# Optimization experiments

Hardware: AMD Instinct MI355X
Metric: run time of the kernel (lower is better)

## Reference

```python
import jax, jax.numpy as jnp
import numpy as np

N, E, F_IN, HID, H, NC, G = 50000, 800000, 128, 64, 4, 64, 128
EPS_BN = 1e-5


def setup_inputs() -> dict:
    key = jax.random.key(0)
    ks = jax.random.split(key, 32)
    inp = {}
    inp['x'] = jax.random.normal(ks[0], (N, F_IN), dtype=jnp.float32)
    inp['edge_index'] = jax.random.randint(ks[1], (2, E), 0, N, dtype=jnp.int32)
    inp['batch'] = jnp.sort(jax.random.randint(ks[2], (N,), 0, G, dtype=jnp.int32))
    dims = [(F_IN, HID, H, True), (HID * H, HID, H, True), (HID * H, NC, 1, False)]
    k = 3
    for li, (fin, c, h, concat) in enumerate(dims):
        out_flat = c * h if concat else c
        inp[f'W{li}'] = jax.random.normal(ks[k], (fin, h * c), dtype=jnp.float32) * (1.0 / np.sqrt(fin)); k += 1
        inp[f'asrc{li}'] = jax.random.normal(ks[k], (h, c), dtype=jnp.float32) * 0.1; k += 1
        inp[f'adst{li}'] = jax.random.normal(ks[k], (h, c), dtype=jnp.float32) * 0.1; k += 1
        inp[f'b{li}'] = jnp.zeros((out_flat,), dtype=jnp.float32)
        inp[f'gamma{li}'] = jnp.ones((out_flat,), dtype=jnp.float32)
        inp[f'beta{li}'] = jnp.zeros((out_flat,), dtype=jnp.float32)
    return inp


def gat_layer(x, src, dst, W, asrc, adst, b, heads, out_ch, concat):
    n = x.shape[0]
    h = (x @ W).reshape(n, heads, out_ch)                      # [N,H,C]
    a_s = jnp.sum(h * asrc, axis=-1)                           # [N,H]
    a_d = jnp.sum(h * adst, axis=-1)                           # [N,H]
    e = jax.nn.leaky_relu(a_s[src] + a_d[dst], 0.2)            # [E',H]
    m = jax.ops.segment_max(e, dst, num_segments=n)            # per-target max
    e = jnp.exp(e - m[dst])
    s = jax.ops.segment_sum(e, dst, num_segments=n)
    alpha = e / (s[dst] + 1e-16)                               # softmax over in-edges
    msg = alpha[:, :, None] * h[src]                           # [E',H,C]
    out = jax.ops.segment_sum(msg, dst, num_segments=n)        # [N,H,C]
    out = out.reshape(n, heads * out_ch) if concat else out.mean(axis=1)
    return out + b


def batchnorm(x, gamma, beta):
    mu = x.mean(axis=0)
    var = x.var(axis=0)  # biased, as torch BN training-mode
    return (x - mu) * jax.lax.rsqrt(var + EPS_BN) * gamma + beta


def reference(x, edge_index, batch, W0, asrc0, adst0, b0, gamma0, beta0,
              W1, asrc1, adst1, b1, gamma1, beta1,
              W2, asrc2, adst2, b2, gamma2, beta2):
    n = x.shape[0]
    loop = jnp.arange(n, dtype=edge_index.dtype)
    src = jnp.concatenate([edge_index[0], loop])  # add self loops (PyG default)
    dst = jnp.concatenate([edge_index[1], loop])
    layers = [(W0, asrc0, adst0, b0, gamma0, beta0, H, HID, True),
              (W1, asrc1, adst1, b1, gamma1, beta1, H, HID, True),
              (W2, asrc2, adst2, b2, gamma2, beta2, 1, NC, False)]
    xs = []
    for (W, asrc, adst, b, gamma, beta, heads, oc, concat) in layers:
        x = jax.nn.elu(gat_layer(x, src, dst, W, asrc, adst, b, heads, oc, concat))
        x = batchnorm(x, gamma, beta)
        xs.append(x)
    x_pool = jnp.concatenate([jax.ops.segment_sum(xx, batch, num_segments=G) for xx in xs], axis=1)
    return (x_pool, jnp.concatenate(xs, axis=1))
```

## Files before the change

kernel.cpp:

```cpp
#include <hip/hip_runtime.h>
#include <math.h>

#define N_NODES 50000
#define NUM_E   800000
#define E_TOT   (NUM_E + N_NODES)
#define M_PAD   50048
#define NGRAPH  128
#define XS_COLS 576
#define EPS_BN  1e-5f

static inline int ceil_div(int a, int b) { return (a + b - 1) / b; }

typedef __attribute__((ext_vector_type(8))) short short8;
typedef __attribute__((ext_vector_type(4))) float f32x4;

__device__ __forceinline__ float bf2f(ushort u) {
    union { unsigned int i; float f; } v; v.i = ((unsigned int)u) << 16; return v.f;
}
__device__ __forceinline__ ushort f2bf(float f) {
    union { float f; unsigned int i; } v; v.f = f;
    unsigned int r = v.i + 0x7FFF + ((v.i >> 16) & 1);
    return (ushort)(r >> 16);
}
__device__ __forceinline__ float lrelu(float l) { return l > 0.f ? l : 0.2f * l; }

__global__ __launch_bounds__(256)
void prep_w(const float* __restrict__ W0, const float* __restrict__ W1,
            const float* __restrict__ W2,
            ushort* __restrict__ Wt0, ushort* __restrict__ Wt1, ushort* __restrict__ Wt2)
{
    int j = blockIdx.x * 256 + threadIdx.x;
    if (j < 256 * 128) { Wt0[j] = f2bf(W0[(size_t)(j % 128) * 256 + (j / 128)]); return; }
    j -= 256 * 128;
    if (j < 256 * 256) { Wt1[j] = f2bf(W1[(size_t)(j % 256) * 256 + (j / 256)]); return; }
    j -= 256 * 256;
    if (j < 64 * 256)  { Wt2[j] = f2bf(W2[(size_t)(j % 256) * 64 + (j / 256)]); }
}

template<bool AF32>
__global__ __launch_bounds__(512)
void gemm_bf16_w(const void* __restrict__ Av, int lda,
                 const ushort* __restrict__ Bt, int ldb,
                 ushort* __restrict__ C, int M, int K,
                 const float* __restrict__ asrc, const float* __restrict__ adst,
                 float* __restrict__ a_s, float* __restrict__ a_d)
{
    __shared__ __align__(16) ushort As[128][64 + 8];
    __shared__ __align__(16) ushort Bs[256][64 + 8];
    const int tid = threadIdx.x;
    const int lane = tid & 63;
    const int w = tid >> 6;
    const int m0 = blockIdx.x * 128;

    f32x4 acc[16] = {};

    for (int k0 = 0; k0 < K; k0 += 64) {
#pragma unroll
        for (int j = 0; j < 2; ++j) {
            int c = tid + j * 512;
            int r = c >> 3, cc = (c & 7) * 8;
            if constexpr (AF32) {
                const float* Af = (const float*)Av;
                int m = m0 + r; if (m >= M) m = M - 1;
                float4 v0 = *reinterpret_cast<const float4*>(Af + (size_t)m * lda + k0 + cc);
                float4 v1 = *reinterpret_cast<const float4*>(Af + (size_t)m * lda + k0 + cc + 4);
                short8 v = {(short)f2bf(v0.x), (short)f2bf(v0.y), (short)f2bf(v0.z), (short)f2bf(v0.w),
                            (short)f2bf(v1.x), (short)f2bf(v1.y), (short)f2bf(v1.z), (short)f2bf(v1.w)};
                *reinterpret_cast<short8*>(&As[r][cc]) = v;
            } else {
                const ushort* Ab = (const ushort*)Av;
                short8 v = *reinterpret_cast<const short8*>(Ab + (size_t)(m0 + r) * lda + k0 + cc);
                *reinterpret_cast<short8*>(&As[r][cc]) = v;
            }
        }
#pragma unroll
        for (int j = 0; j < 4; ++j) {
            int c = tid + j * 512;
            int r = c >> 3, cc = (c & 7) * 8;
            short8 v = *reinterpret_cast<const short8*>(Bt + (size_t)r * ldb + k0 + cc);
            *reinterpret_cast<short8*>(&Bs[r][cc]) = v;
        }
        __syncthreads();
#pragma unroll
        for (int kc = 0; kc < 64; kc += 32) {
            short8 a = *reinterpret_cast<const short8*>(&As[w * 16 + (lane & 15)][kc + (lane >> 4) * 8]);
#pragma unroll
            for (int nf = 0; nf < 16; ++nf) {
                short8 b = *reinterpret_cast<const short8*>(&Bs[nf * 16 + (lane & 15)][kc + (lane >> 4) * 8]);
                acc[nf] = __builtin_amdgcn_mfma_f32_16x16x32_bf16(a, b, acc[nf], 0, 0, 0);
            }
        }
        __syncthreads();
    }

    const int mbase = m0 + w * 16 + (lane >> 4) * 4;
#pragma unroll
    for (int r = 0; r < 4; ++r) {
        int m = mbase + r;
        if (m < M) {
#pragma unroll
            for (int nf = 0; nf < 16; ++nf)
                C[(size_t)m * 256 + nf * 16 + (lane & 15)] = f2bf(acc[nf][r]);
        }
    }

    float asl[16], adl[16];
#pragma unroll
    for (int nf = 0; nf < 16; ++nf) {
        int col = nf * 16 + (lane & 15);
        asl[nf] = asrc[col];
        adl[nf] = adst[col];
    }
#pragma unroll
    for (int r = 0; r < 4; ++r) {
        float ps[4] = {0.f, 0.f, 0.f, 0.f};
        float pd[4] = {0.f, 0.f, 0.f, 0.f};
#pragma unroll
        for (int nf = 0; nf < 16; ++nf) {
            int h = nf >> 2;
            ps[h] = fmaf(acc[nf][r], asl[nf], ps[h]);
            pd[h] = fmaf(acc[nf][r], adl[nf], pd[h]);
        }
#pragma unroll
        for (int h = 0; h < 4; ++h) {
#pragma unroll
            for (int o = 1; o < 16; o <<= 1) {
                ps[h] += __shfl_xor(ps[h], o, 64);
                pd[h] += __shfl_xor(pd[h], o, 64);
            }
        }
        int m = mbase + r;
        if ((lane & 15) == 0 && m < M) {
#pragma unroll
            for (int h = 0; h < 4; ++h) {
                a_s[(size_t)m * 4 + h] = ps[h];
                a_d[(size_t)m * 4 + h] = pd[h];
            }
        }
    }
}

template<int BM, int BN, int BK, int H>
__global__ __launch_bounds__(256)
void gemm_bf16(const ushort* __restrict__ A, int lda,
               const ushort* __restrict__ Bt, int ldb,
               ushort* __restrict__ C, int ldc, int M, int K,
               const float* __restrict__ asrc, const float* __restrict__ adst,
               float* __restrict__ a_s, float* __restrict__ a_d)
{
    static_assert(BM == 128 && BN == 64 && BK == 64, "tuned variant");
    __shared__ __align__(16) ushort As[BM][BK + 8];
    __shared__ __align__(16) ushort Bs[BN][BK + 8];
    const int tid = threadIdx.x;
    const int lane = tid & 63;
    const int w = tid >> 6;
    const int m0 = blockIdx.x * BM;
    const int n0 = blockIdx.y * BN;

    f32x4 acc[2][4] = {};

    for (int k0 = 0; k0 < K; k0 += BK) {
#pragma unroll
        for (int j = 0; j < 4; ++j) {
            int c = tid + j * 256;
            int r = c >> 3, cc = (c & 7) * 8;
            short8 v = *reinterpret_cast<const short8*>(A + (size_t)(m0 + r) * lda + k0 + cc);
            *reinterpret_cast<short8*>(&As[r][cc]) = v;
        }
#pragma unroll
        for (int j = 0; j < 2; ++j) {
            int c = tid + j * 256;
            int r = c >> 3, cc = (c & 7) * 8;
            short8 v = *reinterpret_cast<const short8*>(Bt + (size_t)(n0 + r) * ldb + k0 + cc);
            *reinterpret_cast<short8*>(&Bs[r][cc]) = v;
        }
        __syncthreads();
#pragma unroll
        for (int kc = 0; kc < BK; kc += 32) {
            short8 a[2], b[4];
#pragma unroll
            for (int mf = 0; mf < 2; ++mf)
                a[mf] = *reinterpret_cast<const short8*>(&As[w * 32 + mf * 16 + (lane & 15)][kc + (lane >> 4) * 8]);
#pragma unroll
            for (int nf = 0; nf < 4; ++nf)
                b[nf] = *reinterpret_cast<const short8*>(&Bs[nf * 16 + (lane & 15)][kc + (lane >> 4) * 8]);
#pragma unroll
            for (int mf = 0; mf < 2; ++mf)
#pragma unroll
                for (int nf = 0; nf < 4; ++nf)
                    acc[mf][nf] = __builtin_amdgcn_mfma_f32_16x16x32_bf16(a[mf], b[nf], acc[mf][nf], 0, 0, 0);
        }
        __syncthreads();
    }

#pragma unroll
    for (int mf = 0; mf < 2; ++mf) {
        int mbase = m0 + w * 32 + mf * 16 + (lane >> 4) * 4;
#pragma unroll
        for (int r = 0; r < 4; ++r) {
            int m = mbase + r;
            if (m < M) {
#pragma unroll
                for (int nf = 0; nf < 4; ++nf)
                    C[(size_t)m * ldc + n0 + nf * 16 + (lane & 15)] = f2bf(acc[mf][nf][r]);
            }
        }
    }

    const int hd = blockIdx.y;
    float asl[4], adl[4];
#pragma unroll
    for (int nf = 0; nf < 4; ++nf) {
        int col = n0 + nf * 16 + (lane & 15);
        asl[nf] = asrc[col];
        adl[nf] = adst[col];
    }
#pragma unroll
    for (int mf = 0; mf < 2; ++mf) {
#pragma unroll
        for (int r = 0; r < 4; ++r) {
            float ps = 0.f, pd = 0.f;
#pragma unroll
            for (int nf = 0; nf < 4; ++nf) {
                ps = fmaf(acc[mf][nf][r], asl[nf], ps);
                pd = fmaf(acc[mf][nf][r], adl[nf], pd);
            }
#pragma unroll
            for (int o = 1; o < 16; o <<= 1) {
                ps += __shfl_xor(ps, o, 64);
                pd += __shfl_xor(pd, o, 64);
            }
            int m = m0 + w * 32 + mf * 16 + (lane >> 4) * 4 + r;
            if ((lane & 15) == 0 && m < M) {
                a_s[(size_t)m * H + hd] = ps;
                a_d[(size_t)m * H + hd] = pd;
            }
        }
    }
}

template<int H, int C>
__global__ __launch_bounds__(256)
void gat_fused2(const int* __restrict__ offs, const int* __restrict__ ssrc,
                const float* __restrict__ a_s, const float* __restrict__ a_d,
                const ushort* __restrict__ hf, const float* __restrict__ bias,
                float* __restrict__ out, int ldo)
{
    constexpr int V = (H * C) / 32;
    __shared__ float alsh[4][2][64 * H];
    __shared__ int   ssh[4][2][64];
    const int tid = threadIdx.x;
    const int lane = tid & 63;
    const int wv = tid >> 6;
    const int half = lane >> 5;
    const int ll = lane & 31;
    const int dst = blockIdx.x * 8 + wv * 2 + half;
    if (dst >= N_NODES) return;
    const int e0 = offs[dst], e1 = offs[dst + 1];
    const int deg = e1 - e0;
    const int hd = (ll * V) / C;

    float ad[H];
    if constexpr (H == 4) {
        float4 v = *reinterpret_cast<const float4*>(a_d + (size_t)dst * 4);
        ad[0] = v.x; ad[1] = v.y; ad[2] = v.z; ad[3] = v.w;
    } else ad[0] = a_d[dst];

    float acc[V];
#pragma unroll
    for (int k = 0; k < V; ++k) acc[k] = 0.f;

    if (deg <= 64) {
        const bool a0 = ll < deg;
        const bool a1 = 32 + ll < deg;
        const int s0 = ssrc[e0 + (a0 ? ll : 0)];
        const int s1 = ssrc[e0 + (a1 ? 32 + ll : 0)];
        float l0[H], l1[H], mx[H], sm[H];
        if constexpr (H == 4) {
            float4 v0 = *reinterpret_cast<const float4*>(a_s + (size_t)s0 * 4);
            float4 v1 = *reinterpret_cast<const float4*>(a_s + (size_t)s1 * 4);
            l0[0] = lrelu(v0.x + ad[0]); l0[1] = lrelu(v0.y + ad[1]);
            l0[2] = lrelu(v0.z + ad[2]); l0[3] = lrelu(v0.w + ad[3]);
            l1[0] = lrelu(v1.x + ad[0]); l1[1] = lrelu(v1.y + ad[1]);
            l1[2] = lrelu(v1.z + ad[2]); l1[3] = lrelu(v1.w + ad[3]);
        } else {
            l0[0] = lrelu(a_s[s0] + ad[0]);
            l1[0] = lrelu(a_s[s1] + ad[0]);
        }
#pragma unroll
        for (int t = 0; t < H; ++t) {
            float m = a0 ? l0[t] : -INFINITY;
            if (a1) m = fmaxf(m, l1[t]);
#pragma unroll
            for (int o = 1; o < 32; o <<= 1) m = fmaxf(m, __shfl_xor(m, o, 64));
            mx[t] = m;
            float s = (a0 ? __expf(l0[t] - m) : 0.f) + (a1 ? __expf(l1[t] - m) : 0.f);
#pragma unroll
            for (int o = 1; o < 32; o <<= 1) s += __shfl_xor(s, o, 64);
            sm[t] = s;
        }
        float inv[H];
#pragma unroll
        for (int t = 0; t < H; ++t) inv[t] = 1.f / (sm[t] + 1e-16f);
        if (a0) {
            ssh[wv][half][ll] = s0;
            if constexpr (H == 4) {
                float4 av = {__expf(l0[0] - mx[0]) * inv[0], __expf(l0[1] - mx[1]) * inv[1],
                             __expf(l0[2] - mx[2]) * inv[2], __expf(l0[3] - mx[3]) * inv[3]};
                *reinterpret_cast<float4*>(&alsh[wv][half][ll * 4]) = av;
            } else alsh[wv][half][ll] = __expf(l0[0] - mx[0]) * inv[0];
        }
        if (a1) {
            ssh[wv][half][32 + ll] = s1;
            if constexpr (H == 4) {
                float4 av = {__expf(l1[0] - mx[0]) * inv[0], __expf(l1[1] - mx[1]) * inv[1],
                             __expf(l1[2] - mx[2]) * inv[2], __expf(l1[3] - mx[3]) * inv[3]};
                *reinterpret_cast<float4*>(&alsh[wv][half][(32 + ll) * 4]) = av;
            } else alsh[wv][half][32 + ll] = __expf(l1[0] - mx[0]) * inv[0];
        }

        const ushort* hlane = hf + (size_t)ll * V;
        int j = 0;
        for (; j + 3 < deg; j += 4) {
            int sj[4]; float al[4];
#pragma unroll
            for (int k = 0; k < 4; ++k) {
                sj[k] = ssh[wv][half][j + k];
                al[k] = alsh[wv][half][(j + k) * H + hd];
            }
            if constexpr (V == 8) {
                short8 hv[4];
#pragma unroll
                for (int k = 0; k < 4; ++k)
                    hv[k] = *reinterpret_cast<const short8*>(hlane + (size_t)sj[k] * (H * C));
#pragma unroll
                for (int k = 0; k < 4; ++k)
#pragma unroll
                    for (int i = 0; i < 8; ++i)
                        acc[i] = fmaf(al[k], bf2f((ushort)hv[k][i]), acc[i]);
            } else {
                ushort2 hv[4];
#pragma unroll
                for (int k = 0; k < 4; ++k)
                    hv[k] = *reinterpret_cast<const ushort2*>(hlane + (size_t)sj[k] * (H * C));
#pragma unroll
                for (int k = 0; k < 4; ++k) {
                    acc[0] = fmaf(al[k], bf2f(hv[k].x), acc[0]);
                    acc[1] = fmaf(al[k], bf2f(hv[k].y), acc[1]);
                }
            }
        }
        for (; j < deg; ++j) {
            int sj = ssh[wv][half][j];
            float al = alsh[wv][half][j * H + hd];
            if constexpr (V == 8) {
                short8 hv = *reinterpret_cast<const short8*>(hlane + (size_t)sj * (H * C));
#pragma unroll
                for (int i = 0; i < 8; ++i)
                    acc[i] = fmaf(al, bf2f((ushort)hv[i]), acc[i]);
            } else {
                ushort2 hv = *reinterpret_cast<const ushort2*>(hlane + (size_t)sj * (H * C));
                acc[0] = fmaf(al, bf2f(hv.x), acc[0]);
                acc[1] = fmaf(al, bf2f(hv.y), acc[1]);
            }
        }
    } else {
        float mx[H], sm[H];
#pragma unroll
        for (int t = 0; t < H; ++t) mx[t] = -INFINITY;
        for (int e = e0 + ll; e < e1; e += 32) {
            int s = ssrc[e];
            float asv[H];
            if constexpr (H == 4) {
                float4 v = *reinterpret_cast<const float4*>(a_s + (size_t)s * 4);
                asv[0] = v.x; asv[1] = v.y; asv[2] = v.z; asv[3] = v.w;
            } else asv[0] = a_s[s];
#pragma unroll
            for (int t = 0; t < H; ++t) mx[t] = fmaxf(mx[t], lrelu(asv[t] + ad[t]));
        }
#pragma unroll
        for (int t = 0; t < H; ++t)
#pragma unroll
            for (int o = 1; o < 32; o <<= 1) mx[t] = fmaxf(mx[t], __shfl_xor(mx[t], o, 64));
#pragma unroll
        for (int t = 0; t < H; ++t) sm[t] = 0.f;
        for (int e = e0 + ll; e < e1; e += 32) {
            int s = ssrc[e];
            float asv[H];
            if constexpr (H == 4) {
                float4 v = *reinterpret_cast<const float4*>(a_s + (size_t)s * 4);
                asv[0] = v.x; asv[1] = v.y; asv[2] = v.z; asv[3] = v.w;
            } else asv[0] = a_s[s];
#pragma unroll
            for (int t = 0; t < H; ++t) sm[t] += __expf(lrelu(asv[t] + ad[t]) - mx[t]);
        }
#pragma unroll
        for (int t = 0; t < H; ++t)
#pragma unroll
            for (int o = 1; o < 32; o <<= 1) sm[t] += __shfl_xor(sm[t], o, 64);

        float mxl = mx[0], sml = sm[0], adl = ad[0];
#pragma unroll
        for (int t = 1; t < H; ++t) {
            mxl = (hd == t) ? mx[t] : mxl;
            sml = (hd == t) ? sm[t] : sml;
            adl = (hd == t) ? ad[t] : adl;
        }
        const float invl = 1.f / (sml + 1e-16f);
        const ushort* hlane = hf + (size_t)ll * V;
        for (int e = e0; e < e1; ++e) {
            int s0 = ssrc[e];
            float al0 = __expf(lrelu(a_s[(size_t)s0 * H + hd] + adl) - mxl) * invl;
            if constexpr (V == 8) {
                short8 hv = *reinterpret_cast<const short8*>(hlane + (size_t)s0 * (H * C));
#pragma unroll
                for (int i = 0; i < 8; ++i)
                    acc[i] = fmaf(al0, bf2f((ushort)hv[i]), acc[i]);
            } else {
                ushort2 hv = *reinterpret_cast<const ushort2*>(hlane + (size_t)s0 * (H * C));
                acc[0] = fmaf(al0, bf2f(hv.x), acc[0]);
                acc[1] = fmaf(al0, bf2f(hv.y), acc[1]);
            }
        }
    }

    float res[V];
#pragma unroll
    for (int i = 0; i < V; ++i) {
        float t = acc[i] + bias[ll * V + i];
        res[i] = t > 0.f ? t : (expf(t) - 1.f);
    }
    if constexpr (V == 8) {
        float4 v0 = {res[0], res[1], res[2], res[3]};
        float4 v1 = {res[4], res[5], res[6], res[7]};
        *reinterpret_cast<float4*>(&out[(size_t)dst * ldo + ll * 8 + 0]) = v0;
        *reinterpret_cast<float4*>(&out[(size_t)dst * ldo + ll * 8 + 4]) = v1;
    } else {
        float2 v = {res[0], res[1]};
        *reinterpret_cast<float2*>(&out[(size_t)dst * ldo + ll * 2]) = v;
    }
}

__global__ void edge_count(const int* __restrict__ ei, int* __restrict__ counts)
{
    int i = blockIdx.x * blockDim.x + threadIdx.x;
    if (i >= E_TOT) return;
    int dst = (i < NUM_E) ? ei[NUM_E + i] : (i - NUM_E);
    atomicAdd(&counts[dst], 1);
}

__global__ void edge_scatter(const int* __restrict__ ei, int* __restrict__ cursor,
                             int* __restrict__ ssrc)
{
    int i = blockIdx.x * blockDim.x + threadIdx.x;
    if (i >= E_TOT) return;
    int src, dst;
    if (i < NUM_E) { src = ei[i]; dst = ei[NUM_E + i]; }
    else           { src = dst = i - NUM_E; }
    int pos = atomicAdd(&cursor[dst], 1);
    ssrc[pos] = src;
}

__global__ void scan_block(const int* __restrict__ in, int n,
                           int* __restrict__ incl, int* __restrict__ bsum)
{
    __shared__ int sh[256];
    int tid = threadIdx.x;
    int i = blockIdx.x * 256 + tid;
    int v = (i < n) ? in[i] : 0;
    sh[tid] = v;
    __syncthreads();
    for (int o = 1; o < 256; o <<= 1) {
        int t = (tid >= o) ? sh[tid - o] : 0;
        __syncthreads();
        sh[tid] += t;
        __syncthreads();
    }
    if (i < n) incl[i] = sh[tid];
    if (tid == 255) bsum[blockIdx.x] = sh[255];
}

__global__ void scan_sums(int* __restrict__ bsum, int nb)
{
    __shared__ int sh[256];
    int tid = threadIdx.x;
    int v = (tid < nb) ? bsum[tid] : 0;
    sh[tid] = v;
    __syncthreads();
    for (int o = 1; o < 256; o <<= 1) {
        int t = (tid >= o) ? sh[tid - o] : 0;
        __syncthreads();
        sh[tid] += t;
        __syncthreads();
    }
    if (tid < nb) bsum[tid] = sh[tid] - v;
}

__global__ void scan_final(const int* __restrict__ incl, const int* __restrict__ in,
                           const int* __restrict__ bsum, int n,
                           int* __restrict__ offs, int* __restrict__ cursor)
{
    int i = blockIdx.x * 256 + threadIdx.x;
    if (i >= n) return;
    int excl = incl[i] - in[i] + bsum[i / 256];
    offs[i] = excl;
    cursor[i] = excl;
    if (i == n - 1) offs[n] = incl[i] + bsum[i / 256];
}

template<int OF>
__global__ __launch_bounds__(256)
void bn_stats(const float* __restrict__ x, int ldx, float* __restrict__ part)
{
    constexpr int RP = 256 / OF;
    const int tid = threadIdx.x;
    const int col = tid % OF;
    const int rsub = tid / OF;
    float s = 0.f, s2 = 0.f;
    for (int r = blockIdx.x * RP + rsub; r < N_NODES; r += gridDim.x * RP) {
        float v = x[(size_t)r * ldx + col];
        s += v;
        s2 = fmaf(v, v, s2);
    }
    if constexpr (RP > 1) {
        __shared__ float sh[2][256];
        sh[0][tid] = s; sh[1][tid] = s2;
        __syncthreads();
        if (rsub == 0) {
#pragma unroll
            for (int j = 1; j < RP; ++j) { s += sh[0][col + j * OF]; s2 += sh[1][col + j * OF]; }
        }
    }
    if (rsub == 0) {
        part[(size_t)blockIdx.x * 2 * OF + col] = s;
        part[(size_t)blockIdx.x * 2 * OF + OF + col] = s2;
    }
}

template<int OF>
__global__ void bn_finalize(const float* __restrict__ part, const float* __restrict__ gamma,
                            const float* __restrict__ beta, float* __restrict__ ss)
{
    int c = threadIdx.x;
    if (c >= OF) return;
    float s = 0.f, s2 = 0.f;
    for (int b = 0; b < 256; ++b) {
        s += part[(size_t)b * 2 * OF + c];
        s2 += part[(size_t)b * 2 * OF + OF + c];
    }
    float mean = s / (float)N_NODES;
    float var = s2 / (float)N_NODES - mean * mean;
    float inv = rsqrtf(var + EPS_BN);
    float sc = inv * gamma[c];
    ss[c] = sc;
    ss[OF + c] = beta[c] - mean * sc;
}

template<int OF, bool WB>
__global__ __launch_bounds__(256)
void bn_apply_pool(float* __restrict__ x, int ldx, const float* __restrict__ ss,
                   ushort* __restrict__ xb, int ldxb,
                   const int* __restrict__ batch, float* __restrict__ pool, int poff)
{
    const int tid = threadIdx.x;
    if constexpr (OF == 256) {
        const int c = tid;
        const int r0 = blockIdx.x * 16;
        const float sc = ss[c], sh = ss[OF + c];
        float psum = 0.f;
        int curg = batch[r0];
#pragma unroll
        for (int i = 0; i < 16; ++i) {
            int r = r0 + i;
            int g = batch[r];
            if (g != curg) {
                atomicAdd(&pool[(size_t)curg * XS_COLS + poff + c], psum);
                psum = 0.f; curg = g;
            }
            float v = fmaf(x[(size_t)r * ldx + c], sc, sh);
            x[(size_t)r * ldx + c] = v;
            if constexpr (WB) xb[(size_t)r * ldxb + c] = f2bf(v);
            psum += v;
        }
        atomicAdd(&pool[(size_t)curg * XS_COLS + poff + c], psum);
    } else {
        const int c = tid & 63;
        const int rsub = tid >> 6;
        const int r0 = blockIdx.x * 16;
        const float sc = ss[c], sh = ss[OF + c];
        float psum = 0.f;
        int curg = batch[r0 + rsub];
#pragma unroll
        for (int i = 0; i < 4; ++i) {
            int r = r0 + rsub + i * 4;
            int g = batch[r];
            if (g != curg) {
                atomicAdd(&pool[(size_t)curg * XS_COLS + poff + c], psum);
                psum = 0.f; curg = g;
            }
            float v = fmaf(x[(size_t)r * ldx + c], sc, sh);
            x[(size_t)r * ldx + c] = v;
            if constexpr (WB) xb[(size_t)r * ldxb + c] = f2bf(v);
            psum += v;
        }
        atomicAdd(&pool[(size_t)curg * XS_COLS + poff + c], psum);
    }
}

extern "C" void kernel_launch(void* const* d_in, const int* in_sizes, int n_in,
                              void* d_out, int out_size, void* d_ws, size_t ws_size,
                              hipStream_t stream)
{
    const float* x     = (const float*)d_in[0];
    const int*   ei    = (const int*)d_in[1];
    const int*   batch = (const int*)d_in[2];
    const float* W[3]    = {(const float*)d_in[3],  (const float*)d_in[9],  (const float*)d_in[15]};
    const float* asrc[3] = {(const float*)d_in[4],  (const float*)d_in[10], (const float*)d_in[16]};
    const float* adst[3] = {(const float*)d_in[5],  (const float*)d_in[11], (const float*)d_in[17]};
    const float* bia[3]  = {(const float*)d_in[6],  (const float*)d_in[12], (const float*)d_in[18]};
    const float* gam[3]  = {(const float*)d_in[7],  (const float*)d_in[13], (const float*)d_in[19]};
    const float* bet[3]  = {(const float*)d_in[8],  (const float*)d_in[14], (const float*)d_in[20]};

    char* wp = (char*)d_ws;
    auto alloc = [&](size_t bytes) -> void* {
        void* p = (void*)wp;
        wp += (bytes + 255) & ~(size_t)255;
        return p;
    };
    ushort* hbf   = (ushort*)alloc((size_t)N_NODES * 256 * 2);
    ushort* AbfA  = (ushort*)alloc((size_t)M_PAD * 256 * 2);
    float*  a_s   = (float*)alloc((size_t)N_NODES * 4 * 4);
    float*  a_d   = (float*)alloc((size_t)N_NODES * 4 * 4);
    int*    counts = (int*)alloc((size_t)N_NODES * 4);
    int*    offs   = (int*)alloc((size_t)(N_NODES + 1) * 4);
    int*    cursor = (int*)alloc((size_t)N_NODES * 4);
    int*    incl   = (int*)alloc((size_t)N_NODES * 4);
    int*    bsums  = (int*)alloc(1024);
    int*    ssrc   = (int*)alloc((size_t)E_TOT * 4);
    float*  bnpart = (float*)alloc((size_t)256 * 2 * 256 * 4);
    float*  bnss   = (float*)alloc(2 * 256 * 4);
    ushort* Wt0    = (ushort*)alloc(256 * 128 * 2);
    ushort* Wt1    = (ushort*)alloc(256 * 256 * 2);
    ushort* Wt2    = (ushort*)alloc(64 * 256 * 2);

    float* pool = (float*)d_out;
    float* xs   = pool + (size_t)NGRAPH * XS_COLS;

    hipMemsetAsync(counts, 0, (size_t)N_NODES * 4, stream);
    hipMemsetAsync(pool, 0, (size_t)NGRAPH * XS_COLS * 4, stream);
    edge_count<<<ceil_div(E_TOT, 256), 256, 0, stream>>>(ei, counts);
    const int NSB = ceil_div(N_NODES, 256);
    scan_block<<<NSB, 256, 0, stream>>>(counts, N_NODES, incl, bsums);
    scan_sums<<<1, 256, 0, stream>>>(bsums, NSB);
    scan_final<<<NSB, 256, 0, stream>>>(incl, counts, bsums, N_NODES, offs, cursor);
    edge_scatter<<<ceil_div(E_TOT, 256), 256, 0, stream>>>(ei, cursor, ssrc);
    const int PREP_ITEMS = 256 * 128 + 256 * 256 + 64 * 256;
    prep_w<<<ceil_div(PREP_ITEMS, 256), 256, 0, stream>>>(W[0], W[1], W[2], Wt0, Wt1, Wt2);

    const int NW2 = ceil_div(N_NODES, 8);
    const int NMB = ceil_div(N_NODES, 128);
    const int NBA = N_NODES / 16;

    {
        gemm_bf16_w<true><<<NMB, 512, 0, stream>>>(x, 128, Wt0, 128, hbf, N_NODES, 128,
                                                   asrc[0], adst[0], a_s, a_d);
        gat_fused2<4, 64><<<NW2, 256, 0, stream>>>(offs, ssrc, a_s, a_d, hbf, bia[0], xs + 0, XS_COLS);
        bn_stats<256><<<256, 256, 0, stream>>>(xs + 0, XS_COLS, bnpart);
        bn_finalize<256><<<1, 256, 0, stream>>>(bnpart, gam[0], bet[0], bnss);
        bn_apply_pool<256, true><<<NBA, 256, 0, stream>>>(xs + 0, XS_COLS, bnss, AbfA, 256,
                                                          batch, pool, 0);
    }
    {
        gemm_bf16_w<false><<<NMB, 512, 0, stream>>>(AbfA, 256, Wt1, 256, hbf, N_NODES, 256,
                                                    asrc[1], adst[1], a_s, a_d);
        gat_fused2<4, 64><<<NW2, 256, 0, stream>>>(offs, ssrc, a_s, a_d, hbf, bia[1], xs + 256, XS_COLS);
        bn_stats<256><<<256, 256, 0, stream>>>(xs + 256, XS_COLS, bnpart);
        bn_finalize<256><<<1, 256, 0, stream>>>(bnpart, gam[1], bet[1], bnss);
        bn_apply_pool<256, true><<<NBA, 256, 0, stream>>>(xs + 256, XS_COLS, bnss, AbfA, 256,
                                                          batch, pool, 256);
    }
    {
        dim3 grid(NMB, 1);
        gemm_bf16<128, 64, 64, 1><<<grid, 256, 0, stream>>>(AbfA, 256, Wt2, 256, hbf, 64, N_NODES, 256,
                                                            asrc[2], adst[2], a_s, a_d);
        gat_fused2<1, 64><<<NW2, 256, 0, stream>>>(offs, ssrc, a_s, a_d, hbf, bia[2], xs + 512, XS_COLS);
        bn_stats<64><<<256, 256, 0, stream>>>(xs + 512, XS_COLS, bnpart);
        bn_finalize<64><<<1, 64, 0, stream>>>(bnpart, gam[2], bet[2], bnss);
        bn_apply_pool<64, false><<<NBA, 256, 0, stream>>>(xs + 512, XS_COLS, bnss, nullptr, 0,
                                                          batch, pool, 512);
    }
}
```

Before: 532.8 us.

## Fuse BN statistics into GAT aggregation, stage activations in bf16, merge scan kernels

The GAT aggregation kernel now writes its ELU output as bf16 to a scratch buffer and accumulates per-column sum and sum-of-squares through shared memory. It then issues atomics into 8 slotted partial buffers, which removes the separate bn_stats pass over the fp32 activations. bn_apply_pool reads the bf16 buffer, vectorised two columns per thread, and writes the fp32 output. The scan_sums kernel is folded into scan_final, which reduces the block sums itself. The cost is extra memsets, atomic contention across 8 slots, and BN normalisation applied to bf16-rounded values, which costs precision. The early return for out-of-range dst is also removed, which is safe here because N is a multiple of 8.

```diff
diff --git a/kernel.cpp b/kernel.cpp
--- a/kernel.cpp
+++ b/kernel.cpp
@@ -244,18 +244,20 @@
 void gat_fused2(const int* __restrict__ offs, const int* __restrict__ ssrc,
                 const float* __restrict__ a_s, const float* __restrict__ a_d,
                 const ushort* __restrict__ hf, const float* __restrict__ bias,
-                float* __restrict__ out, int ldo)
+                ushort* __restrict__ ybuf, float* __restrict__ bnsum)
 {
     constexpr int V = (H * C) / 32;
+    constexpr int OF = H * C;
     __shared__ float alsh[4][2][64 * H];
     __shared__ int   ssh[4][2][64];
+    __shared__ float ysh[8][OF];
     const int tid = threadIdx.x;
     const int lane = tid & 63;
     const int wv = tid >> 6;
     const int half = lane >> 5;
     const int ll = lane & 31;
-    const int dst = blockIdx.x * 8 + wv * 2 + half;
-    if (dst >= N_NODES) return;
+    const int dl = wv * 2 + half;
+    const int dst = blockIdx.x * 8 + dl;
     const int e0 = offs[dst], e1 = offs[dst + 1];
     const int deg = e1 - e0;
     const int hd = (ll * V) / C;
@@ -332,7 +334,7 @@
                 short8 hv[4];
 #pragma unroll
                 for (int k = 0; k < 4; ++k)
-                    hv[k] = *reinterpret_cast<const short8*>(hlane + (size_t)sj[k] * (H * C));
+                    hv[k] = *reinterpret_cast<const short8*>(hlane + (size_t)sj[k] * OF);
 #pragma unroll
                 for (int k = 0; k < 4; ++k)
 #pragma unroll
@@ -342,7 +344,7 @@
                 ushort2 hv[4];
 #pragma unroll
                 for (int k = 0; k < 4; ++k)
-                    hv[k] = *reinterpret_cast<const ushort2*>(hlane + (size_t)sj[k] * (H * C));
+                    hv[k] = *reinterpret_cast<const ushort2*>(hlane + (size_t)sj[k] * OF);
 #pragma unroll
                 for (int k = 0; k < 4; ++k) {
                     acc[0] = fmaf(al[k], bf2f(hv[k].x), acc[0]);
@@ -354,12 +356,12 @@
             int sj = ssh[wv][half][j];
             float al = alsh[wv][half][j * H + hd];
             if constexpr (V == 8) {
-                short8 hv = *reinterpret_cast<const short8*>(hlane + (size_t)sj * (H * C));
+                short8 hv = *reinterpret_cast<const short8*>(hlane + (size_t)sj * OF);
 #pragma unroll
                 for (int i = 0; i < 8; ++i)
                     acc[i] = fmaf(al, bf2f((ushort)hv[i]), acc[i]);
             } else {
-                ushort2 hv = *reinterpret_cast<const ushort2*>(hlane + (size_t)sj * (H * C));
+                ushort2 hv = *reinterpret_cast<const ushort2*>(hlane + (size_t)sj * OF);
                 acc[0] = fmaf(al, bf2f(hv.x), acc[0]);
                 acc[1] = fmaf(al, bf2f(hv.y), acc[1]);
             }
@@ -412,12 +414,12 @@
             int s0 = ssrc[e];
             float al0 = __expf(lrelu(a_s[(size_t)s0 * H + hd] + adl) - mxl) * invl;
             if constexpr (V == 8) {
-                short8 hv = *reinterpret_cast<const short8*>(hlane + (size_t)s0 * (H * C));
+                short8 hv = *reinterpret_cast<const short8*>(hlane + (size_t)s0 * OF);
 #pragma unroll
                 for (int i = 0; i < 8; ++i)
                     acc[i] = fmaf(al0, bf2f((ushort)hv[i]), acc[i]);
             } else {
-                ushort2 hv = *reinterpret_cast<const ushort2*>(hlane + (size_t)s0 * (H * C));
+                ushort2 hv = *reinterpret_cast<const ushort2*>(hlane + (size_t)s0 * OF);
                 acc[0] = fmaf(al0, bf2f(hv.x), acc[0]);
                 acc[1] = fmaf(al0, bf2f(hv.y), acc[1]);
             }
@@ -431,13 +433,29 @@
         res[i] = t > 0.f ? t : (expf(t) - 1.f);
     }
     if constexpr (V == 8) {
-        float4 v0 = {res[0], res[1], res[2], res[3]};
-        float4 v1 = {res[4], res[5], res[6], res[7]};
-        *reinterpret_cast<float4*>(&out[(size_t)dst * ldo + ll * 8 + 0]) = v0;
-        *reinterpret_cast<float4*>(&out[(size_t)dst * ldo + ll * 8 + 4]) = v1;
+        short8 yv = {(short)f2bf(res[0]), (short)f2bf(res[1]), (short)f2bf(res[2]), (short)f2bf(res[3]),
+                     (short)f2bf(res[4]), (short)f2bf(res[5]), (short)f2bf(res[6]), (short)f2bf(res[7])};
+        *reinterpret_cast<short8*>(&ybuf[(size_t)dst * OF + ll * 8]) = yv;
+        *reinterpret_cast<f32x4*>(&ysh[dl][ll * 8 + 0]) = f32x4{res[0], res[1], res[2], res[3]};
+        *reinterpret_cast<f32x4*>(&ysh[dl][ll * 8 + 4]) = f32x4{res[4], res[5], res[6], res[7]};
     } else {
-        float2 v = {res[0], res[1]};
-        *reinterpret_cast<float2*>(&out[(size_t)dst * ldo + ll * 2]) = v;
+        ushort2 yv = {f2bf(res[0]), f2bf(res[1])};
+        *reinterpret_cast<ushort2*>(&ybuf[(size_t)dst * OF + ll * 2]) = yv;
+        ysh[dl][ll * 2 + 0] = res[0];
+        ysh[dl][ll * 2 + 1] = res[1];
+    }
+    __syncthreads();
+    if (tid < OF) {
+        float s = 0.f, s2 = 0.f;
+#pragma unroll
+        for (int d = 0; d < 8; ++d) {
+            float v = ysh[d][tid];
+            s += v;
+            s2 = fmaf(v, v, s2);
+        }
+        int slot = blockIdx.x & 7;
+        atomicAdd(&bnsum[(size_t)slot * 2 * OF + tid], s);
+        atomicAdd(&bnsum[(size_t)slot * 2 * OF + OF + tid], s2);
     }
 }
 
@@ -480,73 +498,39 @@
     if (tid == 255) bsum[blockIdx.x] = sh[255];
 }
 
-__global__ void scan_sums(int* __restrict__ bsum, int nb)
-{
-    __shared__ int sh[256];
-    int tid = threadIdx.x;
-    int v = (tid < nb) ? bsum[tid] : 0;
-    sh[tid] = v;
-    __syncthreads();
-    for (int o = 1; o < 256; o <<= 1) {
-        int t = (tid >= o) ? sh[tid - o] : 0;
-        __syncthreads();
-        sh[tid] += t;
-        __syncthreads();
-    }
-    if (tid < nb) bsum[tid] = sh[tid] - v;
-}
-
 __global__ void scan_final(const int* __restrict__ incl, const int* __restrict__ in,
                            const int* __restrict__ bsum, int n,
                            int* __restrict__ offs, int* __restrict__ cursor)
 {
-    int i = blockIdx.x * 256 + threadIdx.x;
+    __shared__ int sh[256];
+    const int tid = threadIdx.x;
+    const int bi = blockIdx.x;
+    sh[tid] = (tid < bi) ? bsum[tid] : 0;
+    __syncthreads();
+    for (int o = 128; o > 0; o >>= 1) {
+        if (tid < o) sh[tid] += sh[tid + o];
+        __syncthreads();
+    }
+    const int pref = sh[0];
+    int i = bi * 256 + tid;
     if (i >= n) return;
-    int excl = incl[i] - in[i] + bsum[i / 256];
+    int excl = incl[i] - in[i] + pref;
     offs[i] = excl;
     cursor[i] = excl;
-    if (i == n - 1) offs[n] = incl[i] + bsum[i / 256];
+    if (i == n - 1) offs[n] = incl[i] + pref;
 }
 
 template<int OF>
-__global__ __launch_bounds__(256)
-void bn_stats(const float* __restrict__ x, int ldx, float* __restrict__ part)
-{
-    constexpr int RP = 256 / OF;
-    const int tid = threadIdx.x;
-    const int col = tid % OF;
-    const int rsub = tid / OF;
-    float s = 0.f, s2 = 0.f;
-    for (int r = blockIdx.x * RP + rsub; r < N_NODES; r += gridDim.x * RP) {
-        float v = x[(size_t)r * ldx + col];
-        s += v;
-        s2 = fmaf(v, v, s2);
-    }
-    if constexpr (RP > 1) {
-        __shared__ float sh[2][256];
-        sh[0][tid] = s; sh[1][tid] = s2;
-        __syncthreads();
-        if (rsub == 0) {
-#pragma unroll
-            for (int j = 1; j < RP; ++j) { s += sh[0][col + j * OF]; s2 += sh[1][col + j * OF]; }
-        }
-    }
-    if (rsub == 0) {
-        part[(size_t)blockIdx.x * 2 * OF + col] = s;
-        part[(size_t)blockIdx.x * 2 * OF + OF + col] = s2;
-    }
-}
-
-template<int OF>
-__global__ void bn_finalize(const float* __restrict__ part, const float* __restrict__ gamma,
+__global__ void bn_finalize(const float* __restrict__ bnsum, const float* __restrict__ gamma,
                             const float* __restrict__ beta, float* __restrict__ ss)
 {
     int c = threadIdx.x;
     if (c >= OF) return;
     float s = 0.f, s2 = 0.f;
-    for (int b = 0; b < 256; ++b) {
-        s += part[(size_t)b * 2 * OF + c];
-        s2 += part[(size_t)b * 2 * OF + OF + c];
+#pragma unroll
+    for (int slot = 0; slot < 8; ++slot) {
+        s += bnsum[(size_t)slot * 2 * OF + c];
+        s2 += bnsum[(size_t)slot * 2 * OF + OF + c];
     }
     float mean = s / (float)N_NODES;
     float var = s2 / (float)N_NODES - mean * mean;
@@ -558,53 +542,42 @@
 
 template<int OF, bool WB>
 __global__ __launch_bounds__(256)
-void bn_apply_pool(float* __restrict__ x, int ldx, const float* __restrict__ ss,
-                   ushort* __restrict__ xb, int ldxb,
+void bn_apply_pool(const ushort* __restrict__ y, float* __restrict__ xs, int ldx,
+                   const float* __restrict__ ss, ushort* __restrict__ xb, int ldxb,
                    const int* __restrict__ batch, float* __restrict__ pool, int poff)
 {
     const int tid = threadIdx.x;
-    if constexpr (OF == 256) {
-        const int c = tid;
-        const int r0 = blockIdx.x * 16;
-        const float sc = ss[c], sh = ss[OF + c];
-        float psum = 0.f;
-        int curg = batch[r0];
-#pragma unroll
-        for (int i = 0; i < 16; ++i) {
-            int r = r0 + i;
-            int g = batch[r];
-            if (g != curg) {
-                atomicAdd(&pool[(size_t)curg * XS_COLS + poff + c], psum);
-                psum = 0.f; curg = g;
-            }
-            float v = fmaf(x[(size_t)r * ldx + c], sc, sh);
-            x[(size_t)r * ldx + c] = v;
-            if constexpr (WB) xb[(size_t)r * ldxb + c] = f2bf(v);
-            psum += v;
-        }
-        atomicAdd(&pool[(size_t)curg * XS_COLS + poff + c], psum);
-    } else {
-        const int c = tid & 63;
-        const int rsub = tid >> 6;
-        const int r0 = blockIdx.x * 16;
-        const float sc = ss[c], sh = ss[OF + c];
-        float psum = 0.f;
-        int curg = batch[r0 + rsub];
-#pragma unroll
-        for (int i = 0; i < 4; ++i) {
-            int r = r0 + rsub + i * 4;
-            int g = batch[r];
-            if (g != curg) {
-                atomicAdd(&pool[(size_t)curg * XS_COLS + poff + c], psum);
-                psum = 0.f; curg = g;
-            }
-            float v = fmaf(x[(size_t)r * ldx + c], sc, sh);
-            x[(size_t)r * ldx + c] = v;
-            if constexpr (WB) xb[(size_t)r * ldxb + c] = f2bf(v);
-            psum += v;
-        }
-        atomicAdd(&pool[(size_t)curg * XS_COLS + poff + c], psum);
-    }
+    constexpr int CP = OF / 2;
+    constexpr int RS = 256 / CP;
+    const int c = (tid % CP) * 2;
+    const int rsub = tid / CP;
+    const int r0 = blockIdx.x * 16;
+    const float sc0 = ss[c], sh0 = ss[OF + c];
+    const float sc1 = ss[c + 1], sh1 = ss[OF + c + 1];
+    float ps0 = 0.f, ps1 = 0.f;
+    int curg = batch[r0 + rsub];
+#pragma unroll
+    for (int i = 0; i < 16 / RS; ++i) {
+        int r = r0 + rsub + i * RS;
+        int g = batch[r];
+        if (g != curg) {
+            atomicAdd(&pool[(size_t)curg * XS_COLS + poff + c], ps0);
+            atomicAdd(&pool[(size_t)curg * XS_COLS + poff + c + 1], ps1);
+            ps0 = ps1 = 0.f; curg = g;
+        }
+        ushort2 hv = *reinterpret_cast<const ushort2*>(y + (size_t)r * OF + c);
+        float v0 = fmaf(bf2f(hv.x), sc0, sh0);
+        float v1 = fmaf(bf2f(hv.y), sc1, sh1);
+        float2 vv = {v0, v1};
+        *reinterpret_cast<float2*>(&xs[(size_t)r * ldx + c]) = vv;
+        if constexpr (WB) {
+            ushort2 bb = {f2bf(v0), f2bf(v1)};
+            *reinterpret_cast<ushort2*>(&xb[(size_t)r * ldxb + c]) = bb;
+        }
+        ps0 += v0; ps1 += v1;
+    }
+    atomicAdd(&pool[(size_t)curg * XS_COLS + poff + c], ps0);
+    atomicAdd(&pool[(size_t)curg * XS_COLS + poff + c + 1], ps1);
 }
 
 extern "C" void kernel_launch(void* const* d_in, const int* in_sizes, int n_in,
@@ -628,6 +601,7 @@
         return p;
     };
     ushort* hbf   = (ushort*)alloc((size_t)N_NODES * 256 * 2);
+    ushort* ybuf  = (ushort*)alloc((size_t)N_NODES * 256 * 2);
     ushort* AbfA  = (ushort*)alloc((size_t)M_PAD * 256 * 2);
     float*  a_s   = (float*)alloc((size_t)N_NODES * 4 * 4);
     float*  a_d   = (float*)alloc((size_t)N_NODES * 4 * 4);
@@ -637,7 +611,7 @@
     int*    incl   = (int*)alloc((size_t)N_NODES * 4);
     int*    bsums  = (int*)alloc(1024);
     int*    ssrc   = (int*)alloc((size_t)E_TOT * 4);
-    float*  bnpart = (float*)alloc((size_t)256 * 2 * 256 * 4);
+    float*  bnsum  = (float*)alloc((size_t)8 * 2 * 256 * 4);
     float*  bnss   = (float*)alloc(2 * 256 * 4);
     ushort* Wt0    = (ushort*)alloc(256 * 128 * 2);
     ushort* Wt1    = (ushort*)alloc(256 * 256 * 2);
@@ -651,7 +625,6 @@
     edge_count<<<ceil_div(E_TOT, 256), 256, 0, stream>>>(ei, counts);
     const int NSB = ceil_div(N_NODES, 256);
     scan_block<<<NSB, 256, 0, stream>>>(counts, N_NODES, incl, bsums);
-    scan_sums<<<1, 256, 0, stream>>>(bsums, NSB);
     scan_final<<<NSB, 256, 0, stream>>>(incl, counts, bsums, N_NODES, offs, cursor);
     edge_scatter<<<ceil_div(E_TOT, 256), 256, 0, stream>>>(ei, cursor, ssrc);
     const int PREP_ITEMS = 256 * 128 + 256 * 256 + 64 * 256;
@@ -664,29 +637,29 @@
     {
         gemm_bf16_w<true><<<NMB, 512, 0, stream>>>(x, 128, Wt0, 128, hbf, N_NODES, 128,
                                                    asrc[0], adst[0], a_s, a_d);
-        gat_fused2<4, 64><<<NW2, 256, 0, stream>>>(offs, ssrc, a_s, a_d, hbf, bia[0], xs + 0, XS_COLS);
-        bn_stats<256><<<256, 256, 0, stream>>>(xs + 0, XS_COLS, bnpart);
-        bn_finalize<256><<<1, 256, 0, stream>>>(bnpart, gam[0], bet[0], bnss);
-        bn_apply_pool<256, true><<<NBA, 256, 0, stream>>>(xs + 0, XS_COLS, bnss, AbfA, 256,
+        hipMemsetAsync(bnsum, 0, (size_t)8 * 2 * 256 * 4, stream);
+        gat_fused2<4, 64><<<NW2, 256, 0, stream>>>(offs, ssrc, a_s, a_d, hbf, bia[0], ybuf, bnsum);
+        bn_finalize<256><<<1, 256, 0, stream>>>(bnsum, gam[0], bet[0], bnss);
+        bn_apply_pool<256, true><<<NBA, 256, 0, stream>>>(ybuf, xs + 0, XS_COLS, bnss, AbfA, 256,
                                                           batch, pool, 0);
     }
     {
         gemm_bf16_w<false><<<NMB, 512, 0, stream>>>(AbfA, 256, Wt1, 256, hbf, N_NODES, 256,
                                                     asrc[1], adst[1], a_s, a_d);
-        gat_fused2<4, 64><<<NW2, 256, 0, stream>>>(offs, ssrc, a_s, a_d, hbf, bia[1], xs + 256, XS_COLS);
-        bn_stats<256><<<256, 256, 0, stream>>>(xs + 256, XS_COLS, bnpart);
-        bn_finalize<256><<<1, 256, 0, stream>>>(bnpart, gam[1], bet[1], bnss);
-        bn_apply_pool<256, true><<<NBA, 256, 0, stream>>>(xs + 256, XS_COLS, bnss, AbfA, 256,
+        hipMemsetAsync(bnsum, 0, (size_t)8 * 2 * 256 * 4, stream);
+        gat_fused2<4, 64><<<NW2, 256, 0, stream>>>(offs, ssrc, a_s, a_d, hbf, bia[1], ybuf, bnsum);
+        bn_finalize<256><<<1, 256, 0, stream>>>(bnsum, gam[1], bet[1], bnss);
+        bn_apply_pool<256, true><<<NBA, 256, 0, stream>>>(ybuf, xs + 256, XS_COLS, bnss, AbfA, 256,
                                                           batch, pool, 256);
     }
     {
         dim3 grid(NMB, 1);
         gemm_bf16<128, 64, 64, 1><<<grid, 256, 0, stream>>>(AbfA, 256, Wt2, 256, hbf, 64, N_NODES, 256,
                                                             asrc[2], adst[2], a_s, a_d);
-        gat_fused2<1, 64><<<NW2, 256, 0, stream>>>(offs, ssrc, a_s, a_d, hbf, bia[2], xs + 512, XS_COLS);
-        bn_stats<64><<<256, 256, 0, stream>>>(xs + 512, XS_COLS, bnpart);
-        bn_finalize<64><<<1, 64, 0, stream>>>(bnpart, gam[2], bet[2], bnss);
-        bn_apply_pool<64, false><<<NBA, 256, 0, stream>>>(xs + 512, XS_COLS, bnss, nullptr, 0,
+        hipMemsetAsync(bnsum, 0, (size_t)8 * 2 * 256 * 4, stream);
+        gat_fused2<1, 64><<<NW2, 256, 0, stream>>>(offs, ssrc, a_s, a_d, hbf, bia[2], ybuf, bnsum);
+        bn_finalize<64><<<1, 64, 0, stream>>>(bnsum, gam[2], bet[2], bnss);
+        bn_apply_pool<64, false><<<NBA, 256, 0, stream>>>(ybuf, xs + 512, XS_COLS, bnss, nullptr, 0,
                                                           batch, pool, 512);
     }
 }
```

New measurement: 461.7 us. -13.3%, faster.
